# Performance work log

Hardware: AMD Instinct MI355X
Metric: run time of the kernel (lower is better)

The kernel has to match this reference:

```python
import jax, jax.numpy as jnp
import numpy as np
from jax import lax

HEAD_NUM = 16
QKV_DIM = 16
TOP_K = 2
SQRT_EMBED = 16.0   # sqrt_embedding_dim for E=256
LOGIT_CLIP = 10.0


def setup_inputs() -> dict:
    key = jax.random.key(0)
    ks = jax.random.split(key, 12)
    B, P, N1, E, HD, NE = 256, 100, 101, 256, 256, 8
    s = 0.05
    return {
        "encoded_last_node": jax.random.normal(ks[0], (B, P, E), jnp.float32),
        "attr": jax.random.uniform(ks[1], (B, P, 4), jnp.float32),
        "encoded_nodes": jax.random.normal(ks[2], (B, N1, E), jnp.float32),
        "ninf_mask": jnp.zeros((B, P, N1), jnp.float32),
        "attention_bias": jax.random.normal(ks[3], (B, P, N1), jnp.float32),
        "attention_bias1": jax.random.normal(ks[4], (B, P, N1), jnp.float32),
        "Wq_last": jax.random.normal(ks[5], (E + 4, HD), jnp.float32) * s,
        "Wk": jax.random.normal(ks[6], (E, HD), jnp.float32) * s,
        "Wv": jax.random.normal(ks[7], (E, HD), jnp.float32) * s,
        "Wg": jax.random.normal(ks[8], (HD, NE), jnp.float32) * s,
        "expert_W": jax.random.normal(ks[9], (NE, HD, E), jnp.float32) * s,
        "expert_b": jnp.zeros((NE, E), jnp.float32),
    }


def _heads(x, H, D):
    B, n, _ = x.shape
    return x.reshape(B, n, H, D).transpose(0, 2, 1, 3)  # (B,H,n,D)


def reference(encoded_last_node, attr, encoded_nodes, ninf_mask,
              attention_bias, attention_bias1, Wq_last, Wk, Wv,
              Wg, expert_W, expert_b):
    B, P, E = encoded_last_node.shape
    H, D = HEAD_NUM, QKV_DIM
    # q from [last_node ; attr], k/v from encoded_nodes (set_kv)
    q = _heads(jnp.concatenate([encoded_last_node, attr], axis=-1) @ Wq_last, H, D)
    k = _heads(encoded_nodes @ Wk, H, D)   # (B,H,N+1,D)
    v = _heads(encoded_nodes @ Wv, H, D)
    inv_sqrt_d = 1.0 / jnp.sqrt(jnp.asarray(D, jnp.float32))
    score = jnp.einsum('bhpd,bhnd->bhpn', q, k) * inv_sqrt_d
    score = score + ninf_mask[:, None, :, :]           # rank3 ninf mask
    w = jax.nn.softmax(score, axis=-1)
    out = jnp.einsum('bhpn,bhnd->bhpd', w, v)
    out_concat = out.transpose(0, 2, 1, 3).reshape(B, P, H * D)
    # --- top-k gated MoE combine (node-level routing, eval path) ---
    x = out_concat.reshape(B * P, H * D)               # tokens
    logits = x @ Wg                                    # (T, NE)
    top_v, top_i = lax.top_k(logits, TOP_K)
    top_g = jax.nn.softmax(top_v, axis=-1)
    gates = jnp.zeros_like(logits).at[
        jnp.arange(x.shape[0])[:, None], top_i].set(top_g)   # (T, NE)
    expert_out = jnp.einsum('tf,efo->teo', x, expert_W) + expert_b[None]
    mh = jnp.einsum('teo,te->to', expert_out, gates).reshape(B, P, E)
    # --- single-head pointer scores with bias + tanh clipping ---
    score2 = jnp.einsum('bpe,bne->bpn', mh, encoded_nodes)
    score2 = score2 + attention_bias + attention_bias1
    score2 = LOGIT_CLIP * jnp.tanh(score2 / SQRT_EMBED)
    probs = jax.nn.softmax(score2 + ninf_mask, axis=-1)  # (B,P,N+1)
    return probs
```

## Files before the change

### kernel.cpp

```cpp
#include <hip/hip_runtime.h>
#include <hip/hip_bf16.h>

#define B   256
#define P   100
#define N1  101
#define E   256
#define HD  256
#define H   16
#define D   16
#define NE  8
#define NTOK (B*P)
#define NKV  (B*N1)

typedef __attribute__((ext_vector_type(8))) short short8;
typedef __attribute__((ext_vector_type(4))) float f32x4;
typedef unsigned short ushort_t;

__device__ __forceinline__ unsigned short f2bf(float f) {
  unsigned int u = __float_as_uint(f);
  unsigned int r = (u + 0x7fffu + ((u >> 16) & 1u)) >> 16;
  return (unsigned short)r;
}
__device__ __forceinline__ float bf2f(unsigned short b) {
  return __uint_as_float(((unsigned int)b) << 16);
}

__global__ __launch_bounds__(256) void wsplit3_kernel(
    const float* __restrict__ W, uint4* __restrict__ Wp, int Kreal) {
  const int gid = blockIdx.x * 256 + threadIdx.x;
  const int lane = gid & 63;
  const int rest = gid >> 6;
  const int gct = rest & 15;
  const int kt = rest >> 4;
  const int k0 = kt * 32 + (lane >> 4) * 8;
  const int c = gct * 16 + (lane & 15);
  unsigned int hw[4], mw[4], lw[4];
#pragma unroll
  for (int jj = 0; jj < 4; ++jj) {
    int ka = k0 + 2 * jj, kb = ka + 1;
    float va = (ka < Kreal) ? W[(size_t)ka * 256 + c] : 0.f;
    float vb = (kb < Kreal) ? W[(size_t)kb * 256 + c] : 0.f;
    unsigned short ha = f2bf(va), hb = f2bf(vb);
    float ra = va - bf2f(ha), rb = vb - bf2f(hb);
    unsigned short ma = f2bf(ra), mb = f2bf(rb);
    unsigned short la = f2bf(ra - bf2f(ma)), lb = f2bf(rb - bf2f(mb));
    hw[jj] = (unsigned int)ha | ((unsigned int)hb << 16);
    mw[jj] = (unsigned int)ma | ((unsigned int)mb << 16);
    lw[jj] = (unsigned int)la | ((unsigned int)lb << 16);
  }
  uint4 uh, um, ul;
  uh.x = hw[0]; uh.y = hw[1]; uh.z = hw[2]; uh.w = hw[3];
  um.x = mw[0]; um.y = mw[1]; um.z = mw[2]; um.w = mw[3];
  ul.x = lw[0]; ul.y = lw[1]; ul.z = lw[2]; ul.w = lw[3];
  Wp[(size_t)(rest * 3 + 0) * 64 + lane] = uh;
  Wp[(size_t)(rest * 3 + 1) * 64 + lane] = um;
  Wp[(size_t)(rest * 3 + 2) * 64 + lane] = ul;
}

template <int KT, int MODE>
__global__ __launch_bounds__(256) void proj3_kernel(
    const float* __restrict__ src, const float* __restrict__ attr,
    const uint4* __restrict__ Wp3, float* __restrict__ outp) {
  const int RSTRIDE = KT * 12 + 1;
  __shared__ uint4 als[32 * (KT * 12 + 1)];
  const int tid = threadIdx.x;
  const int row0 = blockIdx.x * 32;
  const int NKG = KT * 4;
  for (int i = tid; i < 32 * NKG; i += 256) {
    const int row = i / NKG;
    const int kg = i - row * NKG;
    float v[8];
    if (MODE == 0) {
      const float4* s = (const float4*)(src + (size_t)(row0 + row) * 256 + kg * 8);
      float4 x0 = s[0], x1 = s[1];
      v[0] = x0.x; v[1] = x0.y; v[2] = x0.z; v[3] = x0.w;
      v[4] = x1.x; v[5] = x1.y; v[6] = x1.z; v[7] = x1.w;
    } else {
      const int kbase = kg * 8;
      if (kbase < 256) {
        const float4* s = (const float4*)(src + (size_t)(row0 + row) * 256 + kbase);
        float4 x0 = s[0], x1 = s[1];
        v[0] = x0.x; v[1] = x0.y; v[2] = x0.z; v[3] = x0.w;
        v[4] = x1.x; v[5] = x1.y; v[6] = x1.z; v[7] = x1.w;
      } else {
#pragma unroll
        for (int j = 0; j < 8; ++j) {
          int k = kbase + j;
          v[j] = (k >= 256 && k < 260) ? attr[(size_t)(row0 + row) * 4 + (k - 256)]
                                       : 0.f;
        }
      }
    }
    unsigned int hw[4], mw[4], lw[4];
#pragma unroll
    for (int jj = 0; jj < 4; ++jj) {
      float va = v[2 * jj], vb = v[2 * jj + 1];
      unsigned short ha = f2bf(va), hb = f2bf(vb);
      float ra = va - bf2f(ha), rb = vb - bf2f(hb);
      unsigned short ma = f2bf(ra), mb = f2bf(rb);
      unsigned short la = f2bf(ra - bf2f(ma)), lb = f2bf(rb - bf2f(mb));
      hw[jj] = (unsigned int)ha | ((unsigned int)hb << 16);
      mw[jj] = (unsigned int)ma | ((unsigned int)mb << 16);
      lw[jj] = (unsigned int)la | ((unsigned int)lb << 16);
    }
    uint4 uh, um, ul;
    uh.x = hw[0]; uh.y = hw[1]; uh.z = hw[2]; uh.w = hw[3];
    um.x = mw[0]; um.y = mw[1]; um.z = mw[2]; um.w = mw[3];
    ul.x = lw[0]; ul.y = lw[1]; ul.z = lw[2]; ul.w = lw[3];
    const int slot = row * RSTRIDE + kg;
    als[slot] = uh;
    als[slot + NKG] = um;
    als[slot + 2 * NKG] = ul;
  }
  __syncthreads();
  const int w = tid >> 6;
  const int lane = tid & 63;
  const int lr = lane & 15;
  const int lg4 = lane >> 4;
  f32x4 acc[2][4];
#pragma unroll
  for (int rt = 0; rt < 2; ++rt)
#pragma unroll
    for (int ct = 0; ct < 4; ++ct) acc[rt][ct] = (f32x4){0.f, 0.f, 0.f, 0.f};
  for (int kt = 0; kt < KT; ++kt) {
    short8 ah[2], am[2], al[2];
#pragma unroll
    for (int rt = 0; rt < 2; ++rt) {
      const int base = (rt * 16 + lr) * RSTRIDE + kt * 4 + lg4;
      ah[rt] = __builtin_bit_cast(short8, als[base]);
      am[rt] = __builtin_bit_cast(short8, als[base + NKG]);
      al[rt] = __builtin_bit_cast(short8, als[base + 2 * NKG]);
    }
#pragma unroll
    for (int ct = 0; ct < 4; ++ct) {
      const int gct = w * 4 + ct;
      const size_t base = (size_t)((kt * 16 + gct) * 3) * 64 + lane;
      short8 bh = __builtin_bit_cast(short8, Wp3[base]);
      short8 bm = __builtin_bit_cast(short8, Wp3[base + 64]);
      short8 bl = __builtin_bit_cast(short8, Wp3[base + 128]);
#pragma unroll
      for (int rt = 0; rt < 2; ++rt) {
        f32x4 a = acc[rt][ct];
        a = __builtin_amdgcn_mfma_f32_16x16x32_bf16(ah[rt], bh, a, 0, 0, 0);
        a = __builtin_amdgcn_mfma_f32_16x16x32_bf16(ah[rt], bm, a, 0, 0, 0);
        a = __builtin_amdgcn_mfma_f32_16x16x32_bf16(am[rt], bh, a, 0, 0, 0);
        a = __builtin_amdgcn_mfma_f32_16x16x32_bf16(am[rt], bm, a, 0, 0, 0);
        a = __builtin_amdgcn_mfma_f32_16x16x32_bf16(ah[rt], bl, a, 0, 0, 0);
        a = __builtin_amdgcn_mfma_f32_16x16x32_bf16(al[rt], bh, a, 0, 0, 0);
        acc[rt][ct] = a;
      }
    }
  }
#pragma unroll
  for (int rt = 0; rt < 2; ++rt) {
#pragma unroll
    for (int ct = 0; ct < 4; ++ct) {
      const int gct = w * 4 + ct;
#pragma unroll
      for (int reg = 0; reg < 4; ++reg) {
        const int row = row0 + rt * 16 + lg4 * 4 + reg;
        size_t o;
        if (MODE == 0) {
          int bb = row / N1, nn = row - bb * N1;
          o = (((size_t)bb * H + gct) * N1 + nn) * D + lr;
        } else {
          int bb = row / P, pp = row - bb * P;
          o = (((size_t)bb * H + gct) * P + pp) * D + lr;
        }
        outp[o] = acc[rt][ct][reg];
      }
    }
  }
}

__device__ __forceinline__ float dot16(
    const float4& a0, const float4& a1, const float4& a2, const float4& a3,
    const float4& b0, const float4& b1, const float4& b2, const float4& b3) {
  return a0.x * b0.x + a0.y * b0.y + a0.z * b0.z + a0.w * b0.w +
         a1.x * b1.x + a1.y * b1.y + a1.z * b1.z + a1.w * b1.w +
         a2.x * b2.x + a2.y * b2.y + a2.z * b2.z + a2.w * b2.w +
         a3.x * b3.x + a3.y * b3.y + a3.z * b3.z + a3.w * b3.w;
}

__global__ __launch_bounds__(256) void attn_kernel(
    const float* __restrict__ q, const float* __restrict__ k,
    const float* __restrict__ v, const float* __restrict__ ninf,
    float* __restrict__ x) {
  const int b = blockIdx.x >> 2;
  const int h0 = (blockIdx.x & 3) * 4;
  __shared__ float kl[4 * N1 * D];
  __shared__ float vl[4 * N1 * D];
  const int tid = threadIdx.x;
  {
    const float4* ks = (const float4*)(k + ((size_t)b * H + h0) * N1 * D);
    const float4* vs = (const float4*)(v + ((size_t)b * H + h0) * N1 * D);
    float4* kd = (float4*)kl;
    float4* vd = (float4*)vl;
    for (int i = tid; i < N1 * D; i += 256) { kd[i] = ks[i]; vd[i] = vs[i]; }
  }
  const int w = tid >> 6;
  const int lane = tid & 63;
  const int h = h0 + w;
  const int p0 = lane;
  const bool r1 = (lane + 64 < P);
  const int p1 = r1 ? (lane + 64) : (P - 1);
  const float* qb = q + (((size_t)b * H + h) * P) * D;
  float4 qa0 = *(const float4*)&qb[p0 * D + 0];
  float4 qa1 = *(const float4*)&qb[p0 * D + 4];
  float4 qa2 = *(const float4*)&qb[p0 * D + 8];
  float4 qa3 = *(const float4*)&qb[p0 * D + 12];
  float4 qb0 = *(const float4*)&qb[p1 * D + 0];
  float4 qb1 = *(const float4*)&qb[p1 * D + 4];
  float4 qb2 = *(const float4*)&qb[p1 * D + 8];
  float4 qb3 = *(const float4*)&qb[p1 * D + 12];
  const float* m0 = ninf + ((size_t)b * P + p0) * N1;
  const float* m1 = ninf + ((size_t)b * P + p1) * N1;
  const float* kw = kl + w * N1 * D;
  const float* vw = vl + w * N1 * D;
  __syncthreads();

  float mA = -1e30f, mB = -1e30f, lA = 0.f, lB = 0.f;
  float oA[16], oB[16];
#pragma unroll
  for (int d = 0; d < 16; ++d) { oA[d] = 0.f; oB[d] = 0.f; }
  float4 mk0 = *(const float4*)&m0[0];
  float4 mk1 = *(const float4*)&m1[0];
  const float tm0 = m0[100], tm1 = m1[100];

  for (int it = 0; it < 25; ++it) {
    const int n = it * 4;
    const int nn = (it < 24) ? (n + 4) : 0;
    float4 nx0 = *(const float4*)&m0[nn];
    float4 nx1 = *(const float4*)&m1[nn];
    const float4* kr0 = (const float4*)&kw[(n + 0) * D];
    const float4* kr1 = (const float4*)&kw[(n + 1) * D];
    const float4* kr2 = (const float4*)&kw[(n + 2) * D];
    const float4* kr3 = (const float4*)&kw[(n + 3) * D];
    float4 k00 = kr0[0], k01 = kr0[1], k02 = kr0[2], k03 = kr0[3];
    float4 k10 = kr1[0], k11 = kr1[1], k12 = kr1[2], k13 = kr1[3];
    float4 k20 = kr2[0], k21 = kr2[1], k22 = kr2[2], k23 = kr2[3];
    float4 k30 = kr3[0], k31 = kr3[1], k32 = kr3[2], k33 = kr3[3];
    float sA0 = dot16(qa0, qa1, qa2, qa3, k00, k01, k02, k03) * 0.25f + mk0.x;
    float sA1 = dot16(qa0, qa1, qa2, qa3, k10, k11, k12, k13) * 0.25f + mk0.y;
    float sA2 = dot16(qa0, qa1, qa2, qa3, k20, k21, k22, k23) * 0.25f + mk0.z;
    float sA3 = dot16(qa0, qa1, qa2, qa3, k30, k31, k32, k33) * 0.25f + mk0.w;
    float sB0 = dot16(qb0, qb1, qb2, qb3, k00, k01, k02, k03) * 0.25f + mk1.x;
    float sB1 = dot16(qb0, qb1, qb2, qb3, k10, k11, k12, k13) * 0.25f + mk1.y;
    float sB2 = dot16(qb0, qb1, qb2, qb3, k20, k21, k22, k23) * 0.25f + mk1.z;
    float sB3 = dot16(qb0, qb1, qb2, qb3, k30, k31, k32, k33) * 0.25f + mk1.w;
    float mnA = fmaxf(fmaxf(fmaxf(sA0, sA1), fmaxf(sA2, sA3)), mA);
    float mnB = fmaxf(fmaxf(fmaxf(sB0, sB1), fmaxf(sB2, sB3)), mB);
    float scA = __expf(mA - mnA);
    float scB = __expf(mB - mnB);
    float pA0 = __expf(sA0 - mnA), pA1 = __expf(sA1 - mnA);
    float pA2 = __expf(sA2 - mnA), pA3 = __expf(sA3 - mnA);
    float pB0 = __expf(sB0 - mnB), pB1 = __expf(sB1 - mnB);
    float pB2 = __expf(sB2 - mnB), pB3 = __expf(sB3 - mnB);
    lA = lA * scA + (pA0 + pA1) + (pA2 + pA3);
    lB = lB * scB + (pB0 + pB1) + (pB2 + pB3);
    const float4* vr0 = (const float4*)&vw[(n + 0) * D];
    const float4* vr1 = (const float4*)&vw[(n + 1) * D];
    const float4* vr2 = (const float4*)&vw[(n + 2) * D];
    const float4* vr3 = (const float4*)&vw[(n + 3) * D];
#pragma unroll
    for (int dq = 0; dq < 4; ++dq) {
      float4 v0 = vr0[dq], v1 = vr1[dq], v2 = vr2[dq], v3 = vr3[dq];
      oA[4 * dq + 0] = oA[4 * dq + 0] * scA + pA0 * v0.x + pA1 * v1.x + pA2 * v2.x + pA3 * v3.x;
      oA[4 * dq + 1] = oA[4 * dq + 1] * scA + pA0 * v0.y + pA1 * v1.y + pA2 * v2.y + pA3 * v3.y;
      oA[4 * dq + 2] = oA[4 * dq + 2] * scA + pA0 * v0.z + pA1 * v1.z + pA2 * v2.z + pA3 * v3.z;
      oA[4 * dq + 3] = oA[4 * dq + 3] * scA + pA0 * v0.w + pA1 * v1.w + pA2 * v2.w + pA3 * v3.w;
      oB[4 * dq + 0] = oB[4 * dq + 0] * scB + pB0 * v0.x + pB1 * v1.x + pB2 * v2.x + pB3 * v3.x;
      oB[4 * dq + 1] = oB[4 * dq + 1] * scB + pB0 * v0.y + pB1 * v1.y + pB2 * v2.y + pB3 * v3.y;
      oB[4 * dq + 2] = oB[4 * dq + 2] * scB + pB0 * v0.z + pB1 * v1.z + pB2 * v2.z + pB3 * v3.z;
      oB[4 * dq + 3] = oB[4 * dq + 3] * scB + pB0 * v0.w + pB1 * v1.w + pB2 * v2.w + pB3 * v3.w;
    }
    mA = mnA; mB = mnB;
    mk0 = nx0; mk1 = nx1;
  }
  {
    const float4* kr = (const float4*)&kw[100 * D];
    float4 k0 = kr[0], k1 = kr[1], k2 = kr[2], k3 = kr[3];
    float sA = dot16(qa0, qa1, qa2, qa3, k0, k1, k2, k3) * 0.25f + tm0;
    float sB = dot16(qb0, qb1, qb2, qb3, k0, k1, k2, k3) * 0.25f + tm1;
    float mnA = fmaxf(mA, sA), mnB = fmaxf(mB, sB);
    float scA = __expf(mA - mnA), scB = __expf(mB - mnB);
    float pA = __expf(sA - mnA), pB = __expf(sB - mnB);
    lA = lA * scA + pA;
    lB = lB * scB + pB;
    const float4* vr = (const float4*)&vw[100 * D];
#pragma unroll
    for (int dq = 0; dq < 4; ++dq) {
      float4 v0 = vr[dq];
      oA[4 * dq + 0] = oA[4 * dq + 0] * scA + pA * v0.x;
      oA[4 * dq + 1] = oA[4 * dq + 1] * scA + pA * v0.y;
      oA[4 * dq + 2] = oA[4 * dq + 2] * scA + pA * v0.z;
      oA[4 * dq + 3] = oA[4 * dq + 3] * scA + pA * v0.w;
      oB[4 * dq + 0] = oB[4 * dq + 0] * scB + pB * v0.x;
      oB[4 * dq + 1] = oB[4 * dq + 1] * scB + pB * v0.y;
      oB[4 * dq + 2] = oB[4 * dq + 2] * scB + pB * v0.z;
      oB[4 * dq + 3] = oB[4 * dq + 3] * scB + pB * v0.w;
    }
  }
  const float invA = 1.f / lA;
  float* xr0 = &x[((size_t)b * P + p0) * HD + h * D];
#pragma unroll
  for (int dq = 0; dq < 4; ++dq) {
    float4 t;
    t.x = oA[4 * dq + 0] * invA; t.y = oA[4 * dq + 1] * invA;
    t.z = oA[4 * dq + 2] * invA; t.w = oA[4 * dq + 3] * invA;
    *(float4*)&xr0[4 * dq] = t;
  }
  if (r1) {
    const float invB = 1.f / lB;
    float* xr1 = &x[((size_t)b * P + p1) * HD + h * D];
#pragma unroll
    for (int dq = 0; dq < 4; ++dq) {
      float4 t;
      t.x = oB[4 * dq + 0] * invB; t.y = oB[4 * dq + 1] * invB;
      t.z = oB[4 * dq + 2] * invB; t.w = oB[4 * dq + 3] * invB;
      *(float4*)&xr1[4 * dq] = t;
    }
  }
}

__global__ __launch_bounds__(256) void logits_top2_kernel(
    const float* __restrict__ x, const float* __restrict__ Wg,
    int* __restrict__ topi, float* __restrict__ topg,
    ushort_t* __restrict__ xsplit) {
  __shared__ float xl[32][260];
  __shared__ float wg[E * NE];
  __shared__ float lg[32][9];
  const int tid = threadIdx.x;
  const int t0 = blockIdx.x * 32;
  for (int r = 0; r < 32; ++r) {
    float val = x[(size_t)(t0 + r) * HD + tid];
    xl[r][tid] = val;
    unsigned short hi = f2bf(val);
    unsigned short lo = f2bf(val - bf2f(hi));
    xsplit[(size_t)(t0 + r) * 512 + tid] = hi;
    xsplit[(size_t)(t0 + r) * 512 + 256 + tid] = lo;
  }
  for (int i = tid; i < E * NE; i += 256) wg[i] = Wg[i];
  __syncthreads();
  const int r = tid >> 3, e = tid & 7;
  float acc = 0.f;
  for (int f = 0; f < E; ++f) acc += xl[r][f] * wg[f * NE + e];
  lg[r][e] = acc;
  __syncthreads();
  if (tid < 32) {
    float v[8];
#pragma unroll
    for (int j = 0; j < 8; ++j) v[j] = lg[tid][j];
    int i1 = 0; float v1 = v[0];
#pragma unroll
    for (int j = 1; j < 8; ++j) if (v[j] > v1) { v1 = v[j]; i1 = j; }
    int i2 = -1; float v2 = -1e30f;
#pragma unroll
    for (int j = 0; j < 8; ++j)
      if (j != i1 && v[j] > v2) { v2 = v[j]; i2 = j; }
    float ex = __expf(v2 - v1);
    float g1 = 1.f / (1.f + ex);
    float g2 = ex / (1.f + ex);
    int t = t0 + tid;
    topi[t * 2 + 0] = i1; topi[t * 2 + 1] = i2;
    topg[t * 2 + 0] = g1; topg[t * 2 + 1] = g2;
  }
}

__global__ __launch_bounds__(1024) void build_lists_kernel(
    const int* __restrict__ topi, const float* __restrict__ topg,
    int* __restrict__ list_tok, float* __restrict__ list_gate,
    int* __restrict__ counts) {
  const int e = blockIdx.x;
  const int tid = threadIdx.x;
  const int lane = tid & 63, w = tid >> 6;
  __shared__ int wsum[16];
  int running = 0;
  for (int c = 0; c < NTOK; c += 1024) {
    int t = c + tid;
    int ia = topi[t * 2 + 0], ib = topi[t * 2 + 1];
    int slot = (ia == e) ? 0 : ((ib == e) ? 1 : -1);
    int f = (slot >= 0) ? 1 : 0;
    unsigned long long m = __ballot(f);
    if (lane == 0) wsum[w] = __popcll(m);
    __syncthreads();
    int wbase = 0, total = 0;
#pragma unroll
    for (int i = 0; i < 16; ++i) {
      int s = wsum[i];
      if (i < w) wbase += s;
      total += s;
    }
    if (f) {
      int prefix = __popcll(m & ((1ull << lane) - 1ull));
      int pos = running + wbase + prefix;
      list_tok[e * NTOK + pos] = (t << 1) | slot;
      list_gate[e * NTOK + pos] = topg[t * 2 + slot];
    }
    running += total;
    __syncthreads();
  }
  if (tid == 0) counts[e] = running;
}

__global__ __launch_bounds__(256) void wsplit_kernel(
    const float* __restrict__ eW, uint4* __restrict__ Wp) {
  const int gid = blockIdx.x * 256 + threadIdx.x;
  const int lane = gid & 63;
  const int rest = gid >> 6;
  const int gct = rest & 15;
  const int kt = (rest >> 4) & 7;
  const int e = rest >> 7;
  const int kbase = kt * 32 + (lane >> 4) * 8;
  const int c = gct * 16 + (lane & 15);
  unsigned int hi[4], lo[4];
#pragma unroll
  for (int jj = 0; jj < 4; ++jj) {
    float v0 = eW[((size_t)e * HD + (kbase + 2 * jj)) * E + c];
    float v1 = eW[((size_t)e * HD + (kbase + 2 * jj + 1)) * E + c];
    unsigned short h0 = f2bf(v0), h1 = f2bf(v1);
    unsigned short l0 = f2bf(v0 - bf2f(h0)), l1 = f2bf(v1 - bf2f(h1));
    hi[jj] = (unsigned int)h0 | ((unsigned int)h1 << 16);
    lo[jj] = (unsigned int)l0 | ((unsigned int)l1 << 16);
  }
  uint4 uh, ul;
  uh.x = hi[0]; uh.y = hi[1]; uh.z = hi[2]; uh.w = hi[3];
  ul.x = lo[0]; ul.y = lo[1]; ul.z = lo[2]; ul.w = lo[3];
  Wp[(size_t)(rest * 2 + 0) * 64 + lane] = uh;
  Wp[(size_t)(rest * 2 + 1) * 64 + lane] = ul;
}

__global__ __launch_bounds__(256) void expert_gemm_kernel(
    const ushort_t* __restrict__ xsplit, const uint4* __restrict__ Wp,
    const float* __restrict__ eb, const int* __restrict__ list_tok,
    const float* __restrict__ list_gate, const int* __restrict__ counts,
    float* __restrict__ p0, float* __restrict__ p1) {
  int e = 0, t0 = -1;
  {
    int rem = blockIdx.x;
    for (int i = 0; i < NE; ++i) {
      int nt = (counts[i] + 31) >> 5;
      if (rem < nt) { e = i; t0 = rem * 32; break; }
      rem -= nt;
    }
  }
  if (t0 < 0) return;
  const int cnt = counts[e];
  const int nr = min(32, cnt - t0);
  __shared__ uint4 xls[32 * 65];
  __shared__ int stok[32];
  __shared__ float sg[32];
  const int tid = threadIdx.x;
  if (tid < 32) {
    int src = e * NTOK + t0 + ((tid < nr) ? tid : 0);
    stok[tid] = list_tok[src];
    sg[tid] = (tid < nr) ? list_gate[e * NTOK + t0 + tid] : 0.f;
  }
  __syncthreads();
  for (int i = tid; i < 32 * 64; i += 256) {
    int r = i >> 6, ch = i & 63;
    const uint4* src = (const uint4*)(xsplit + (size_t)(stok[r] >> 1) * 512);
    xls[r * 65 + ch] = src[ch];
  }
  __syncthreads();
  const int w = tid >> 6;
  const int lane = tid & 63;
  const int lr = lane & 15;
  const int lg4 = lane >> 4;
  f32x4 acc[2][4];
#pragma unroll
  for (int rt = 0; rt < 2; ++rt)
#pragma unroll
    for (int ct = 0; ct < 4; ++ct) acc[rt][ct] = (f32x4){0.f, 0.f, 0.f, 0.f};

  for (int kt = 0; kt < 8; ++kt) {
    short8 afrag[2][2];
#pragma unroll
    for (int rt = 0; rt < 2; ++rt)
#pragma unroll
      for (int pl = 0; pl < 2; ++pl) {
        uint4 u = xls[(rt * 16 + lr) * 65 + pl * 32 + kt * 4 + lg4];
        afrag[rt][pl] = __builtin_bit_cast(short8, u);
      }
#pragma unroll
    for (int ct = 0; ct < 4; ++ct) {
      const int gct = w * 4 + ct;
      const size_t base = (size_t)(((e * 8 + kt) * 16 + gct) * 2) * 64 + lane;
      short8 bh = __builtin_bit_cast(short8, Wp[base]);
      short8 bl = __builtin_bit_cast(short8, Wp[base + 64]);
#pragma unroll
      for (int rt = 0; rt < 2; ++rt) {
        acc[rt][ct] = __builtin_amdgcn_mfma_f32_16x16x32_bf16(
            afrag[rt][0], bh, acc[rt][ct], 0, 0, 0);
        acc[rt][ct] = __builtin_amdgcn_mfma_f32_16x16x32_bf16(
            afrag[rt][0], bl, acc[rt][ct], 0, 0, 0);
        acc[rt][ct] = __builtin_amdgcn_mfma_f32_16x16x32_bf16(
            afrag[rt][1], bh, acc[rt][ct], 0, 0, 0);
      }
    }
  }
#pragma unroll
  for (int rt = 0; rt < 2; ++rt) {
#pragma unroll
    for (int ct = 0; ct < 4; ++ct) {
      const int col = (w * 4 + ct) * 16 + lr;
      const float bias = eb[e * E + col];
#pragma unroll
      for (int reg = 0; reg < 4; ++reg) {
        const int ridx = rt * 16 + lg4 * 4 + reg;
        if (ridx < nr) {
          const int tokw = stok[ridx];
          const float g = sg[ridx];
          float* dst = ((tokw & 1) ? p1 : p0) + (size_t)(tokw >> 1) * E + col;
          *dst = g * (acc[rt][ct][reg] + bias);
        }
      }
    }
  }
}

__global__ __launch_bounds__(128) void score2_kernel(
    const float* __restrict__ p0, const float* __restrict__ p1,
    const float* __restrict__ enc, float* __restrict__ out) {
  const int b = blockIdx.y;
  const int pt = blockIdx.x * 25;
  __shared__ float mh[25][E];
  const int tid = threadIdx.x;
  for (int i = tid; i < 25 * E; i += 128) {
    int r = i >> 8, c = i & 255;
    int t = b * P + pt + r;
    mh[r][c] = p0[(size_t)t * E + c] + p1[(size_t)t * E + c];
  }
  __syncthreads();
  const int n = tid;
  if (n >= N1) return;
  float acc[25];
#pragma unroll
  for (int r = 0; r < 25; ++r) acc[r] = 0.f;
  const float* er = enc + ((size_t)b * N1 + n) * E;
  for (int ee = 0; ee < E; ee += 4) {
    float4 ev = *(const float4*)&er[ee];
#pragma unroll
    for (int r = 0; r < 25; ++r) {
      float4 mv = *(const float4*)&mh[r][ee];
      acc[r] += mv.x * ev.x + mv.y * ev.y + mv.z * ev.z + mv.w * ev.w;
    }
  }
#pragma unroll
  for (int r = 0; r < 25; ++r) out[((size_t)b * P + pt + r) * N1 + n] = acc[r];
}

__global__ __launch_bounds__(256) void softmax2_kernel(
    float* __restrict__ sc, const float* __restrict__ ab,
    const float* __restrict__ ab1, const float* __restrict__ ninf) {
  const int row = blockIdx.x * 4 + (threadIdx.x >> 6);
  const int lane = threadIdx.x & 63;
  float* srow = sc + (size_t)row * N1;
  const float* a = ab + (size_t)row * N1;
  const float* a1 = ab1 + (size_t)row * N1;
  const float* nf = ninf + (size_t)row * N1;
  float s0 = -1e30f, s1 = -1e30f;
  {
    int i = lane;
    float s = srow[i] + a[i] + a1[i];
    float e2 = __expf(s * 0.125f);
    float th = 1.f - 2.f / (e2 + 1.f);
    s0 = 10.f * th + nf[i];
  }
  if (lane < N1 - 64) {
    int i = lane + 64;
    float s = srow[i] + a[i] + a1[i];
    float e2 = __expf(s * 0.125f);
    float th = 1.f - 2.f / (e2 + 1.f);
    s1 = 10.f * th + nf[i];
  }
  float mx = fmaxf(s0, s1);
#pragma unroll
  for (int off = 32; off > 0; off >>= 1) mx = fmaxf(mx, __shfl_xor(mx, off, 64));
  float p0 = __expf(s0 - mx);
  float p1 = (lane < N1 - 64) ? __expf(s1 - mx) : 0.f;
  float sum = p0 + p1;
#pragma unroll
  for (int off = 32; off > 0; off >>= 1) sum += __shfl_xor(sum, off, 64);
  float inv = 1.f / sum;
  srow[lane] = p0 * inv;
  if (lane < N1 - 64) srow[lane + 64] = p1 * inv;
}

extern "C" void kernel_launch(void* const* d_in, const int* in_sizes, int n_in,
                              void* d_out, int out_size, void* d_ws,
                              size_t ws_size, hipStream_t stream) {
  const float* eln  = (const float*)d_in[0];
  const float* attr = (const float*)d_in[1];
  const float* enc  = (const float*)d_in[2];
  const float* ninf = (const float*)d_in[3];
  const float* ab   = (const float*)d_in[4];
  const float* ab1  = (const float*)d_in[5];
  const float* Wq   = (const float*)d_in[6];
  const float* Wk   = (const float*)d_in[7];
  const float* Wv   = (const float*)d_in[8];
  const float* Wg   = (const float*)d_in[9];
  const float* eW   = (const float*)d_in[10];
  const float* eb   = (const float*)d_in[11];
  float* out = (float*)d_out;

  char* ws = (char*)d_ws;
  size_t off = 0;
  auto carve = [&](size_t bytes) {
    char* p = ws + off;
    off += (bytes + 255) & ~size_t(255);
    return p;
  };
  float* kbuf = (float*)carve(sizeof(float) * NKV * HD);
  float* vbuf = (float*)carve(sizeof(float) * NKV * HD);
  float* qbuf = (float*)carve(sizeof(float) * NTOK * HD);
  float* xbuf = (float*)carve(sizeof(float) * NTOK * HD);
  int*   topi = (int*)carve(sizeof(int) * NTOK * 2);
  float* topg = (float*)carve(sizeof(float) * NTOK * 2);
  int*   counts = (int*)carve(sizeof(int) * 16);
  int*   list_tok = (int*)carve(sizeof(int) * NE * NTOK);
  float* list_gate = (float*)carve(sizeof(float) * NE * NTOK);
  uint4* Wp  = (uint4*)carve(sizeof(ushort_t) * NE * HD * E * 2);
  uint4* Wk3 = (uint4*)carve((size_t)8 * 16 * 3 * 64 * 16);
  uint4* Wv3 = (uint4*)carve((size_t)8 * 16 * 3 * 64 * 16);
  uint4* Wq3 = (uint4*)carve((size_t)9 * 16 * 3 * 64 * 16);
  float* pp0 = kbuf;
  float* pp1 = vbuf;
  ushort_t* xsplit = (ushort_t*)qbuf;

  wsplit_kernel<<<256, 256, 0, stream>>>(eW, Wp);
  wsplit3_kernel<<<32, 256, 0, stream>>>(Wk, Wk3, 256);
  wsplit3_kernel<<<32, 256, 0, stream>>>(Wv, Wv3, 256);
  wsplit3_kernel<<<36, 256, 0, stream>>>(Wq, Wq3, 260);
  proj3_kernel<8, 0><<<NKV / 32, 256, 0, stream>>>(enc, nullptr, Wk3, kbuf);
  proj3_kernel<8, 0><<<NKV / 32, 256, 0, stream>>>(enc, nullptr, Wv3, vbuf);
  proj3_kernel<9, 1><<<NTOK / 32, 256, 0, stream>>>(eln, attr, Wq3, qbuf);
  attn_kernel<<<B * 4, 256, 0, stream>>>(qbuf, kbuf, vbuf, ninf, xbuf);
  logits_top2_kernel<<<NTOK / 32, 256, 0, stream>>>(xbuf, Wg, topi, topg,
                                                    xsplit);
  build_lists_kernel<<<NE, 1024, 0, stream>>>(topi, topg, list_tok, list_gate,
                                              counts);
  expert_gemm_kernel<<<1608, 256, 0, stream>>>(xsplit, Wp, eb, list_tok,
                                               list_gate, counts, pp0, pp1);
  dim3 s2(4, B);
  score2_kernel<<<s2, 128, 0, stream>>>(pp0, pp1, enc, out);
  softmax2_kernel<<<NTOK / 4, 256, 0, stream>>>(out, ab, ab1, ninf);
}
```

Measured before the change: 336.6 us.

## Fuse K/V projections into one kernel and split attention over query halves

Merges the separate K and V projection launches into one kernel that converts the encoded_nodes tile to bf16 split form once and feeds both weight sets, so the input read and conversion are not done twice. The attention kernel now launches twice as many blocks, each handling one half of the queries with one query per lane. V is read straight from global memory instead of shared memory, which halves shared memory per block. The softmax uses exp2 with the scale and log2e folded into q, and the dot products are written as explicit fmaf chains. This trades duplicated K staging across the two half-blocks, plus uncached global V reads, for higher occupancy and less register pressure.

```diff
diff --git a/kernel.cpp b/kernel.cpp
--- a/kernel.cpp
+++ b/kernel.cpp
@@ -55,6 +55,127 @@
   Wp[(size_t)(rest * 3 + 0) * 64 + lane] = uh;
   Wp[(size_t)(rest * 3 + 1) * 64 + lane] = um;
   Wp[(size_t)(rest * 3 + 2) * 64 + lane] = ul;
+}
+
+__device__ __forceinline__ void split3_pack(const float* v, uint4& uh,
+                                            uint4& um, uint4& ul) {
+  unsigned int hw[4], mw[4], lw[4];
+#pragma unroll
+  for (int jj = 0; jj < 4; ++jj) {
+    float va = v[2 * jj], vb = v[2 * jj + 1];
+    unsigned short ha = f2bf(va), hb = f2bf(vb);
+    float ra = va - bf2f(ha), rb = vb - bf2f(hb);
+    unsigned short ma = f2bf(ra), mb = f2bf(rb);
+    unsigned short la = f2bf(ra - bf2f(ma)), lb = f2bf(rb - bf2f(mb));
+    hw[jj] = (unsigned int)ha | ((unsigned int)hb << 16);
+    mw[jj] = (unsigned int)ma | ((unsigned int)mb << 16);
+    lw[jj] = (unsigned int)la | ((unsigned int)lb << 16);
+  }
+  uh.x = hw[0]; uh.y = hw[1]; uh.z = hw[2]; uh.w = hw[3];
+  um.x = mw[0]; um.y = mw[1]; um.z = mw[2]; um.w = mw[3];
+  ul.x = lw[0]; ul.y = lw[1]; ul.z = lw[2]; ul.w = lw[3];
+}
+
+__global__ __launch_bounds__(256) void kvproj3_kernel(
+    const float* __restrict__ enc, const uint4* __restrict__ Wk3,
+    const uint4* __restrict__ Wv3, float* __restrict__ kout,
+    float* __restrict__ vout) {
+  const int KT = 8;
+  const int NKG = KT * 4;
+  const int RSTRIDE = KT * 12 + 1;
+  __shared__ uint4 als[32 * 97];
+  const int tid = threadIdx.x;
+  const int row0 = blockIdx.x * 32;
+  for (int i = tid; i < 32 * NKG; i += 256) {
+    const int row = i >> 5;
+    const int kg = i & 31;
+    float v[8];
+    const float4* s = (const float4*)(enc + (size_t)(row0 + row) * 256 + kg * 8);
+    float4 x0 = s[0], x1 = s[1];
+    v[0] = x0.x; v[1] = x0.y; v[2] = x0.z; v[3] = x0.w;
+    v[4] = x1.x; v[5] = x1.y; v[6] = x1.z; v[7] = x1.w;
+    uint4 uh, um, ul;
+    split3_pack(v, uh, um, ul);
+    const int slot = row * RSTRIDE + kg;
+    als[slot] = uh;
+    als[slot + NKG] = um;
+    als[slot + 2 * NKG] = ul;
+  }
+  __syncthreads();
+  const int w = tid >> 6;
+  const int lane = tid & 63;
+  const int lr = lane & 15;
+  const int lg4 = lane >> 4;
+  f32x4 acck[2][4], accv[2][4];
+#pragma unroll
+  for (int rt = 0; rt < 2; ++rt)
+#pragma unroll
+    for (int ct = 0; ct < 4; ++ct) {
+      acck[rt][ct] = (f32x4){0.f, 0.f, 0.f, 0.f};
+      accv[rt][ct] = (f32x4){0.f, 0.f, 0.f, 0.f};
+    }
+  for (int kt = 0; kt < KT; ++kt) {
+    short8 ah[2], am[2], al[2];
+#pragma unroll
+    for (int rt = 0; rt < 2; ++rt) {
+      const int base = (rt * 16 + lr) * RSTRIDE + kt * 4 + lg4;
+      ah[rt] = __builtin_bit_cast(short8, als[base]);
+      am[rt] = __builtin_bit_cast(short8, als[base + NKG]);
+      al[rt] = __builtin_bit_cast(short8, als[base + 2 * NKG]);
+    }
+#pragma unroll
+    for (int ct = 0; ct < 4; ++ct) {
+      const int gct = w * 4 + ct;
+      const size_t base = (size_t)((kt * 16 + gct) * 3) * 64 + lane;
+      {
+        short8 bh = __builtin_bit_cast(short8, Wk3[base]);
+        short8 bm = __builtin_bit_cast(short8, Wk3[base + 64]);
+        short8 bl = __builtin_bit_cast(short8, Wk3[base + 128]);
+#pragma unroll
+        for (int rt = 0; rt < 2; ++rt) {
+          f32x4 a = acck[rt][ct];
+          a = __builtin_amdgcn_mfma_f32_16x16x32_bf16(ah[rt], bh, a, 0, 0, 0);
+          a = __builtin_amdgcn_mfma_f32_16x16x32_bf16(ah[rt], bm, a, 0, 0, 0);
+          a = __builtin_amdgcn_mfma_f32_16x16x32_bf16(am[rt], bh, a, 0, 0, 0);
+          a = __builtin_amdgcn_mfma_f32_16x16x32_bf16(am[rt], bm, a, 0, 0, 0);
+          a = __builtin_amdgcn_mfma_f32_16x16x32_bf16(ah[rt], bl, a, 0, 0, 0);
+          a = __builtin_amdgcn_mfma_f32_16x16x32_bf16(al[rt], bh, a, 0, 0, 0);
+          acck[rt][ct] = a;
+        }
+      }
+      {
+        short8 bh = __builtin_bit_cast(short8, Wv3[base]);
+        short8 bm = __builtin_bit_cast(short8, Wv3[base + 64]);
+        short8 bl = __builtin_bit_cast(short8, Wv3[base + 128]);
+#pragma unroll
+        for (int rt = 0; rt < 2; ++rt) {
+          f32x4 a = accv[rt][ct];
+          a = __builtin_amdgcn_mfma_f32_16x16x32_bf16(ah[rt], bh, a, 0, 0, 0);
+          a = __builtin_amdgcn_mfma_f32_16x16x32_bf16(ah[rt], bm, a, 0, 0, 0);
+          a = __builtin_amdgcn_mfma_f32_16x16x32_bf16(am[rt], bh, a, 0, 0, 0);
+          a = __builtin_amdgcn_mfma_f32_16x16x32_bf16(am[rt], bm, a, 0, 0, 0);
+          a = __builtin_amdgcn_mfma_f32_16x16x32_bf16(ah[rt], bl, a, 0, 0, 0);
+          a = __builtin_amdgcn_mfma_f32_16x16x32_bf16(al[rt], bh, a, 0, 0, 0);
+          accv[rt][ct] = a;
+        }
+      }
+    }
+  }
+#pragma unroll
+  for (int rt = 0; rt < 2; ++rt) {
+#pragma unroll
+    for (int ct = 0; ct < 4; ++ct) {
+      const int gct = w * 4 + ct;
+#pragma unroll
+      for (int reg = 0; reg < 4; ++reg) {
+        const int row = row0 + rt * 16 + lg4 * 4 + reg;
+        int bb = row / N1, nn = row - bb * N1;
+        size_t o = (((size_t)bb * H + gct) * N1 + nn) * D + lr;
+        kout[o] = acck[rt][ct][reg];
+        vout[o] = accv[rt][ct][reg];
+      }
+    }
+  }
 }
 
 template <int KT, int MODE>
@@ -70,43 +191,22 @@
     const int row = i / NKG;
     const int kg = i - row * NKG;
     float v[8];
-    if (MODE == 0) {
-      const float4* s = (const float4*)(src + (size_t)(row0 + row) * 256 + kg * 8);
+    const int kbase = kg * 8;
+    if (MODE == 0 || kbase < 256) {
+      const float4* s = (const float4*)(src + (size_t)(row0 + row) * 256 + kbase);
       float4 x0 = s[0], x1 = s[1];
       v[0] = x0.x; v[1] = x0.y; v[2] = x0.z; v[3] = x0.w;
       v[4] = x1.x; v[5] = x1.y; v[6] = x1.z; v[7] = x1.w;
     } else {
-      const int kbase = kg * 8;
-      if (kbase < 256) {
-        const float4* s = (const float4*)(src + (size_t)(row0 + row) * 256 + kbase);
-        float4 x0 = s[0], x1 = s[1];
-        v[0] = x0.x; v[1] = x0.y; v[2] = x0.z; v[3] = x0.w;
-        v[4] = x1.x; v[5] = x1.y; v[6] = x1.z; v[7] = x1.w;
-      } else {
-#pragma unroll
-        for (int j = 0; j < 8; ++j) {
-          int k = kbase + j;
-          v[j] = (k >= 256 && k < 260) ? attr[(size_t)(row0 + row) * 4 + (k - 256)]
-                                       : 0.f;
-        }
-      }
-    }
-    unsigned int hw[4], mw[4], lw[4];
-#pragma unroll
-    for (int jj = 0; jj < 4; ++jj) {
-      float va = v[2 * jj], vb = v[2 * jj + 1];
-      unsigned short ha = f2bf(va), hb = f2bf(vb);
-      float ra = va - bf2f(ha), rb = vb - bf2f(hb);
-      unsigned short ma = f2bf(ra), mb = f2bf(rb);
-      unsigned short la = f2bf(ra - bf2f(ma)), lb = f2bf(rb - bf2f(mb));
-      hw[jj] = (unsigned int)ha | ((unsigned int)hb << 16);
-      mw[jj] = (unsigned int)ma | ((unsigned int)mb << 16);
-      lw[jj] = (unsigned int)la | ((unsigned int)lb << 16);
+#pragma unroll
+      for (int j = 0; j < 8; ++j) {
+        int k = kbase + j;
+        v[j] = (k >= 256 && k < 260) ? attr[(size_t)(row0 + row) * 4 + (k - 256)]
+                                     : 0.f;
+      }
     }
     uint4 uh, um, ul;
-    uh.x = hw[0]; uh.y = hw[1]; uh.z = hw[2]; uh.w = hw[3];
-    um.x = mw[0]; um.y = mw[1]; um.z = mw[2]; um.w = mw[3];
-    ul.x = lw[0]; ul.y = lw[1]; ul.z = lw[2]; ul.w = lw[3];
+    split3_pack(v, uh, um, ul);
     const int slot = row * RSTRIDE + kg;
     als[slot] = uh;
     als[slot + NKG] = um;
@@ -173,65 +273,68 @@
   }
 }
 
-__device__ __forceinline__ float dot16(
+__device__ __forceinline__ float dot16f(
     const float4& a0, const float4& a1, const float4& a2, const float4& a3,
     const float4& b0, const float4& b1, const float4& b2, const float4& b3) {
-  return a0.x * b0.x + a0.y * b0.y + a0.z * b0.z + a0.w * b0.w +
-         a1.x * b1.x + a1.y * b1.y + a1.z * b1.z + a1.w * b1.w +
-         a2.x * b2.x + a2.y * b2.y + a2.z * b2.z + a2.w * b2.w +
-         a3.x * b3.x + a3.y * b3.y + a3.z * b3.z + a3.w * b3.w;
+  float s = a0.x * b0.x;
+  s = fmaf(a0.y, b0.y, s); s = fmaf(a0.z, b0.z, s); s = fmaf(a0.w, b0.w, s);
+  s = fmaf(a1.x, b1.x, s); s = fmaf(a1.y, b1.y, s); s = fmaf(a1.z, b1.z, s);
+  s = fmaf(a1.w, b1.w, s);
+  s = fmaf(a2.x, b2.x, s); s = fmaf(a2.y, b2.y, s); s = fmaf(a2.z, b2.z, s);
+  s = fmaf(a2.w, b2.w, s);
+  s = fmaf(a3.x, b3.x, s); s = fmaf(a3.y, b3.y, s); s = fmaf(a3.z, b3.z, s);
+  s = fmaf(a3.w, b3.w, s);
+  return s;
 }
 
 __global__ __launch_bounds__(256) void attn_kernel(
     const float* __restrict__ q, const float* __restrict__ k,
     const float* __restrict__ v, const float* __restrict__ ninf,
     float* __restrict__ x) {
-  const int b = blockIdx.x >> 2;
-  const int h0 = (blockIdx.x & 3) * 4;
+  const int b = blockIdx.x >> 3;
+  const int hq = (blockIdx.x >> 1) & 3;
+  const int half = blockIdx.x & 1;
+  const int h0 = hq * 4;
   __shared__ float kl[4 * N1 * D];
-  __shared__ float vl[4 * N1 * D];
   const int tid = threadIdx.x;
   {
     const float4* ks = (const float4*)(k + ((size_t)b * H + h0) * N1 * D);
-    const float4* vs = (const float4*)(v + ((size_t)b * H + h0) * N1 * D);
     float4* kd = (float4*)kl;
-    float4* vd = (float4*)vl;
-    for (int i = tid; i < N1 * D; i += 256) { kd[i] = ks[i]; vd[i] = vs[i]; }
+    for (int i = tid; i < N1 * D; i += 256) kd[i] = ks[i];
   }
   const int w = tid >> 6;
   const int lane = tid & 63;
   const int h = h0 + w;
-  const int p0 = lane;
-  const bool r1 = (lane + 64 < P);
-  const int p1 = r1 ? (lane + 64) : (P - 1);
-  const float* qb = q + (((size_t)b * H + h) * P) * D;
-  float4 qa0 = *(const float4*)&qb[p0 * D + 0];
-  float4 qa1 = *(const float4*)&qb[p0 * D + 4];
-  float4 qa2 = *(const float4*)&qb[p0 * D + 8];
-  float4 qa3 = *(const float4*)&qb[p0 * D + 12];
-  float4 qb0 = *(const float4*)&qb[p1 * D + 0];
-  float4 qb1 = *(const float4*)&qb[p1 * D + 4];
-  float4 qb2 = *(const float4*)&qb[p1 * D + 8];
-  float4 qb3 = *(const float4*)&qb[p1 * D + 12];
-  const float* m0 = ninf + ((size_t)b * P + p0) * N1;
-  const float* m1 = ninf + ((size_t)b * P + p1) * N1;
+  const int prow = half * 64 + lane;
+  const bool act = (prow < P);
+  const int p = act ? prow : (P - 1);
+  const float LOG2E = 1.4426950408889634f;
+  const float c1 = 0.25f * LOG2E;
+  const float* qb = q + (((size_t)b * H + h) * P + p) * D;
+  float4 qa0 = *(const float4*)&qb[0];
+  float4 qa1 = *(const float4*)&qb[4];
+  float4 qa2 = *(const float4*)&qb[8];
+  float4 qa3 = *(const float4*)&qb[12];
+  qa0.x *= c1; qa0.y *= c1; qa0.z *= c1; qa0.w *= c1;
+  qa1.x *= c1; qa1.y *= c1; qa1.z *= c1; qa1.w *= c1;
+  qa2.x *= c1; qa2.y *= c1; qa2.z *= c1; qa2.w *= c1;
+  qa3.x *= c1; qa3.y *= c1; qa3.z *= c1; qa3.w *= c1;
+  const float* mrow = ninf + ((size_t)b * P + p) * N1;
   const float* kw = kl + w * N1 * D;
-  const float* vw = vl + w * N1 * D;
+  const float* vg = v + ((size_t)b * H + h) * N1 * D;
   __syncthreads();
 
-  float mA = -1e30f, mB = -1e30f, lA = 0.f, lB = 0.f;
-  float oA[16], oB[16];
-#pragma unroll
-  for (int d = 0; d < 16; ++d) { oA[d] = 0.f; oB[d] = 0.f; }
-  float4 mk0 = *(const float4*)&m0[0];
-  float4 mk1 = *(const float4*)&m1[0];
-  const float tm0 = m0[100], tm1 = m1[100];
+  float m2 = -1e30f, l = 0.f;
+  float o[16];
+#pragma unroll
+  for (int d = 0; d < 16; ++d) o[d] = 0.f;
+  float4 mk = *(const float4*)&mrow[0];
+  const float tmask = mrow[100];
 
   for (int it = 0; it < 25; ++it) {
     const int n = it * 4;
     const int nn = (it < 24) ? (n + 4) : 0;
-    float4 nx0 = *(const float4*)&m0[nn];
-    float4 nx1 = *(const float4*)&m1[nn];
+    float4 nx = *(const float4*)&mrow[nn];
     const float4* kr0 = (const float4*)&kw[(n + 0) * D];
     const float4* kr1 = (const float4*)&kw[(n + 1) * D];
     const float4* kr2 = (const float4*)&kw[(n + 2) * D];
@@ -240,85 +343,61 @@
     float4 k10 = kr1[0], k11 = kr1[1], k12 = kr1[2], k13 = kr1[3];
     float4 k20 = kr2[0], k21 = kr2[1], k22 = kr2[2], k23 = kr2[3];
     float4 k30 = kr3[0], k31 = kr3[1], k32 = kr3[2], k33 = kr3[3];
-    float sA0 = dot16(qa0, qa1, qa2, qa3, k00, k01, k02, k03) * 0.25f + mk0.x;
-    float sA1 = dot16(qa0, qa1, qa2, qa3, k10, k11, k12, k13) * 0.25f + mk0.y;
-    float sA2 = dot16(qa0, qa1, qa2, qa3, k20, k21, k22, k23) * 0.25f + mk0.z;
-    float sA3 = dot16(qa0, qa1, qa2, qa3, k30, k31, k32, k33) * 0.25f + mk0.w;
-    float sB0 = dot16(qb0, qb1, qb2, qb3, k00, k01, k02, k03) * 0.25f + mk1.x;
-    float sB1 = dot16(qb0, qb1, qb2, qb3, k10, k11, k12, k13) * 0.25f + mk1.y;
-    float sB2 = dot16(qb0, qb1, qb2, qb3, k20, k21, k22, k23) * 0.25f + mk1.z;
-    float sB3 = dot16(qb0, qb1, qb2, qb3, k30, k31, k32, k33) * 0.25f + mk1.w;
-    float mnA = fmaxf(fmaxf(fmaxf(sA0, sA1), fmaxf(sA2, sA3)), mA);
-    float mnB = fmaxf(fmaxf(fmaxf(sB0, sB1), fmaxf(sB2, sB3)), mB);
-    float scA = __expf(mA - mnA);
-    float scB = __expf(mB - mnB);
-    float pA0 = __expf(sA0 - mnA), pA1 = __expf(sA1 - mnA);
-    float pA2 = __expf(sA2 - mnA), pA3 = __expf(sA3 - mnA);
-    float pB0 = __expf(sB0 - mnB), pB1 = __expf(sB1 - mnB);
-    float pB2 = __expf(sB2 - mnB), pB3 = __expf(sB3 - mnB);
-    lA = lA * scA + (pA0 + pA1) + (pA2 + pA3);
-    lB = lB * scB + (pB0 + pB1) + (pB2 + pB3);
-    const float4* vr0 = (const float4*)&vw[(n + 0) * D];
-    const float4* vr1 = (const float4*)&vw[(n + 1) * D];
-    const float4* vr2 = (const float4*)&vw[(n + 2) * D];
-    const float4* vr3 = (const float4*)&vw[(n + 3) * D];
+    float s0 = fmaf(mk.x, LOG2E, dot16f(qa0, qa1, qa2, qa3, k00, k01, k02, k03));
+    float s1 = fmaf(mk.y, LOG2E, dot16f(qa0, qa1, qa2, qa3, k10, k11, k12, k13));
+    float s2 = fmaf(mk.z, LOG2E, dot16f(qa0, qa1, qa2, qa3, k20, k21, k22, k23));
+    float s3 = fmaf(mk.w, LOG2E, dot16f(qa0, qa1, qa2, qa3, k30, k31, k32, k33));
+    float mn = fmaf(0.f, 0.f, fmaxf(fmaxf(fmaxf(s0, s1), fmaxf(s2, s3)), m2));
+    float sc = exp2f(m2 - mn);
+    float p0 = exp2f(s0 - mn), p1 = exp2f(s1 - mn);
+    float p2 = exp2f(s2 - mn), p3 = exp2f(s3 - mn);
+    l = fmaf(l, sc, (p0 + p1) + (p2 + p3));
+    const float4* vr0 = (const float4*)&vg[(n + 0) * D];
+    const float4* vr1 = (const float4*)&vg[(n + 1) * D];
+    const float4* vr2 = (const float4*)&vg[(n + 2) * D];
+    const float4* vr3 = (const float4*)&vg[(n + 3) * D];
 #pragma unroll
     for (int dq = 0; dq < 4; ++dq) {
       float4 v0 = vr0[dq], v1 = vr1[dq], v2 = vr2[dq], v3 = vr3[dq];
-      oA[4 * dq + 0] = oA[4 * dq + 0] * scA + pA0 * v0.x + pA1 * v1.x + pA2 * v2.x + pA3 * v3.x;
-      oA[4 * dq + 1] = oA[4 * dq + 1] * scA + pA0 * v0.y + pA1 * v1.y + pA2 * v2.y + pA3 * v3.y;
-      oA[4 * dq + 2] = oA[4 * dq + 2] * scA + pA0 * v0.z + pA1 * v1.z + pA2 * v2.z + pA3 * v3.z;
-      oA[4 * dq + 3] = oA[4 * dq + 3] * scA + pA0 * v0.w + pA1 * v1.w + pA2 * v2.w + pA3 * v3.w;
-      oB[4 * dq + 0] = oB[4 * dq + 0] * scB + pB0 * v0.x + pB1 * v1.x + pB2 * v2.x + pB3 * v3.x;
-      oB[4 * dq + 1] = oB[4 * dq + 1] * scB + pB0 * v0.y + pB1 * v1.y + pB2 * v2.y + pB3 * v3.y;
-      oB[4 * dq + 2] = oB[4 * dq + 2] * scB + pB0 * v0.z + pB1 * v1.z + pB2 * v2.z + pB3 * v3.z;
-      oB[4 * dq + 3] = oB[4 * dq + 3] * scB + pB0 * v0.w + pB1 * v1.w + pB2 * v2.w + pB3 * v3.w;
-    }
-    mA = mnA; mB = mnB;
-    mk0 = nx0; mk1 = nx1;
+      o[4 * dq + 0] = fmaf(o[4 * dq + 0], sc,
+          fmaf(p0, v0.x, fmaf(p1, v1.x, fmaf(p2, v2.x, p3 * v3.x))));
+      o[4 * dq + 1] = fmaf(o[4 * dq + 1], sc,
+          fmaf(p0, v0.y, fmaf(p1, v1.y, fmaf(p2, v2.y, p3 * v3.y))));
+      o[4 * dq + 2] = fmaf(o[4 * dq + 2], sc,
+          fmaf(p0, v0.z, fmaf(p1, v1.z, fmaf(p2, v2.z, p3 * v3.z))));
+      o[4 * dq + 3] = fmaf(o[4 * dq + 3], sc,
+          fmaf(p0, v0.w, fmaf(p1, v1.w, fmaf(p2, v2.w, p3 * v3.w))));
+    }
+    m2 = mn;
+    mk = nx;
   }
   {
     const float4* kr = (const float4*)&kw[100 * D];
     float4 k0 = kr[0], k1 = kr[1], k2 = kr[2], k3 = kr[3];
-    float sA = dot16(qa0, qa1, qa2, qa3, k0, k1, k2, k3) * 0.25f + tm0;
-    float sB = dot16(qb0, qb1, qb2, qb3, k0, k1, k2, k3) * 0.25f + tm1;
-    float mnA = fmaxf(mA, sA), mnB = fmaxf(mB, sB);
-    float scA = __expf(mA - mnA), scB = __expf(mB - mnB);
-    float pA = __expf(sA - mnA), pB = __expf(sB - mnB);
-    lA = lA * scA + pA;
-    lB = lB * scB + pB;
-    const float4* vr = (const float4*)&vw[100 * D];
+    float s = fmaf(tmask, LOG2E, dot16f(qa0, qa1, qa2, qa3, k0, k1, k2, k3));
+    float mn = fmaxf(m2, s);
+    float sc = exp2f(m2 - mn);
+    float pp = exp2f(s - mn);
+    l = fmaf(l, sc, pp);
+    const float4* vr = (const float4*)&vg[100 * D];
 #pragma unroll
     for (int dq = 0; dq < 4; ++dq) {
       float4 v0 = vr[dq];
-      oA[4 * dq + 0] = oA[4 * dq + 0] * scA + pA * v0.x;
-      oA[4 * dq + 1] = oA[4 * dq + 1] * scA + pA * v0.y;
-      oA[4 * dq + 2] = oA[4 * dq + 2] * scA + pA * v0.z;
-      oA[4 * dq + 3] = oA[4 * dq + 3] * scA + pA * v0.w;
-      oB[4 * dq + 0] = oB[4 * dq + 0] * scB + pB * v0.x;
-      oB[4 * dq + 1] = oB[4 * dq + 1] * scB + pB * v0.y;
-      oB[4 * dq + 2] = oB[4 * dq + 2] * scB + pB * v0.z;
-      oB[4 * dq + 3] = oB[4 * dq + 3] * scB + pB * v0.w;
-    }
-  }
-  const float invA = 1.f / lA;
-  float* xr0 = &x[((size_t)b * P + p0) * HD + h * D];
-#pragma unroll
-  for (int dq = 0; dq < 4; ++dq) {
-    float4 t;
-    t.x = oA[4 * dq + 0] * invA; t.y = oA[4 * dq + 1] * invA;
-    t.z = oA[4 * dq + 2] * invA; t.w = oA[4 * dq + 3] * invA;
-    *(float4*)&xr0[4 * dq] = t;
-  }
-  if (r1) {
-    const float invB = 1.f / lB;
-    float* xr1 = &x[((size_t)b * P + p1) * HD + h * D];
+      o[4 * dq + 0] = fmaf(o[4 * dq + 0], sc, pp * v0.x);
+      o[4 * dq + 1] = fmaf(o[4 * dq + 1], sc, pp * v0.y);
+      o[4 * dq + 2] = fmaf(o[4 * dq + 2], sc, pp * v0.z);
+      o[4 * dq + 3] = fmaf(o[4 * dq + 3], sc, pp * v0.w);
+    }
+  }
+  if (act) {
+    const float inv = 1.f / l;
+    float* xr = &x[((size_t)b * P + p) * HD + h * D];
 #pragma unroll
     for (int dq = 0; dq < 4; ++dq) {
       float4 t;
-      t.x = oB[4 * dq + 0] * invB; t.y = oB[4 * dq + 1] * invB;
-      t.z = oB[4 * dq + 2] * invB; t.w = oB[4 * dq + 3] * invB;
-      *(float4*)&xr1[4 * dq] = t;
+      t.x = o[4 * dq + 0] * inv; t.y = o[4 * dq + 1] * inv;
+      t.z = o[4 * dq + 2] * inv; t.w = o[4 * dq + 3] * inv;
+      *(float4*)&xr[4 * dq] = t;
     }
   }
 }
@@ -632,10 +711,9 @@
   wsplit3_kernel<<<32, 256, 0, stream>>>(Wk, Wk3, 256);
   wsplit3_kernel<<<32, 256, 0, stream>>>(Wv, Wv3, 256);
   wsplit3_kernel<<<36, 256, 0, stream>>>(Wq, Wq3, 260);
-  proj3_kernel<8, 0><<<NKV / 32, 256, 0, stream>>>(enc, nullptr, Wk3, kbuf);
-  proj3_kernel<8, 0><<<NKV / 32, 256, 0, stream>>>(enc, nullptr, Wv3, vbuf);
+  kvproj3_kernel<<<NKV / 32, 256, 0, stream>>>(enc, Wk3, Wv3, kbuf, vbuf);
   proj3_kernel<9, 1><<<NTOK / 32, 256, 0, stream>>>(eln, attr, Wq3, qbuf);
-  attn_kernel<<<B * 4, 256, 0, stream>>>(qbuf, kbuf, vbuf, ninf, xbuf);
+  attn_kernel<<<B * 8, 256, 0, stream>>>(qbuf, kbuf, vbuf, ninf, xbuf);
   logits_top2_kernel<<<NTOK / 32, 256, 0, stream>>>(xbuf, Wg, topi, topg,
                                                     xsplit);
   build_lists_kernel<<<NE, 1024, 0, stream>>>(topi, topg, list_tok, list_gate,
```

New measurement: 456.6 us. +35.7%, slower.
